# Optimization experiments

Measured on AMD Instinct MI355X. Metric: run time of the kernel, lower is better.

Reference implementation:

```python
import jax, jax.numpy as jnp
import numpy as np

B, N = 64, 8192
RW_APPROX_THRES = 0.6
L_CUTOFF = 100
EPS = 1e-12


def _skew(k):
    kx, ky, kz = k[..., 0], k[..., 1], k[..., 2]
    z = jnp.zeros_like(kx)
    return jnp.stack([
        jnp.stack([z, -kz, ky], -1),
        jnp.stack([kz, z, -kx], -1),
        jnp.stack([-ky, kx, z], -1)], -2)


def so3_exp(v):
    # v: [..., 3] rotation vector -> [..., 3, 3] rotation matrix (Rodrigues)
    theta = jnp.linalg.norm(v, axis=-1, keepdims=True)
    k = v / jnp.maximum(theta, 1e-12)
    K = _skew(k)
    s = jnp.sin(theta)[..., None]
    c = jnp.cos(theta)[..., None]
    I = jnp.eye(3, dtype=v.dtype)
    return I + s * K + (1.0 - c) * (K @ K)


def so3_log(r):
    # r: [..., 3, 3] rotation matrix -> [..., 3] rotation vector
    tr = r[..., 0, 0] + r[..., 1, 1] + r[..., 2, 2]
    cos = jnp.clip((tr - 1.0) * 0.5, -1.0 + 1e-7, 1.0 - 1e-7)
    theta = jnp.arccos(cos)  # [...]
    a = jnp.stack([
        r[..., 2, 1] - r[..., 1, 2],
        r[..., 0, 2] - r[..., 2, 0],
        r[..., 1, 0] - r[..., 0, 1]], axis=-1)  # [..., 3]
    scale = theta / (2.0 * jnp.sin(theta))
    return a * scale[..., None]


def igso3_grad_log_pdf(sigma, omega):
    # sigma: [B], omega: [B, N] angles in (0, pi)
    # f(w) = sum_l (2l+1) exp(-l(l+1) sigma^2 / 2) sin((l+1/2) w) / sin(w/2)
    l = jnp.arange(L_CUTOFF + 1, dtype=omega.dtype)          # [L]
    s2 = (sigma ** 2)[:, None, None]                          # [B,1,1]
    coef = (2.0 * l + 1.0) * jnp.exp(-l * (l + 1.0) * s2 / 2.0)  # [B,1,L]
    w = omega[..., None]                                      # [B,N,1]
    lh = l + 0.5
    sin_h = jnp.sin(w / 2.0)
    cos_h = jnp.cos(w / 2.0)
    sin_lw = jnp.sin(lh * w)                                  # [B,N,L]
    f = jnp.sum(coef * sin_lw / sin_h, axis=-1)               # [B,N]
    df = jnp.sum(coef * (lh * jnp.cos(lh * w) * sin_h - 0.5 * cos_h * sin_lw) / (sin_h ** 2), axis=-1)
    return df / (f + EPS)


def setup_inputs() -> dict:
    key = jax.random.key(0)
    k1, k2, k3, k4, k5 = jax.random.split(key, 5)
    ax1 = jax.random.normal(k1, (B, N, 3), dtype=jnp.float32)
    ax1 = ax1 / jnp.linalg.norm(ax1, axis=-1, keepdims=True)
    ang1 = jax.random.uniform(k2, (B, N, 1), minval=0.1, maxval=3.0, dtype=jnp.float32)
    r_t = so3_exp(ax1 * ang1)
    ax2 = jax.random.normal(k3, (B, N, 3), dtype=jnp.float32)
    ax2 = ax2 / jnp.linalg.norm(ax2, axis=-1, keepdims=True)
    ang2 = jax.random.uniform(k4, (B, N, 1), minval=0.1, maxval=3.0, dtype=jnp.float32)
    rh_0 = so3_exp(ax2 * ang2)
    sigma_t = jax.random.uniform(k5, (B,), minval=0.7, maxval=2.5, dtype=jnp.float32)
    return {"r_t": r_t, "rh_0": rh_0, "sigma_t": sigma_t}


def reference(r_t, rh_0, sigma_t):
    # RotationDiffuser.score with left=True
    r_z = jnp.einsum('bnij,bnkj->bnik', r_t, rh_0)  # r_t @ rh_0^T
    v_z = so3_log(r_z)                               # [B,N,3]
    rw_approx = -v_z / (sigma_t[:, None, None] ** 2)
    w = jnp.linalg.norm(v_z, axis=-1)                # [B,N]
    dlogf_dw = igso3_grad_log_pdf(sigma_t, w)        # [B,N]
    score = jnp.where(sigma_t[:, None, None] > RW_APPROX_THRES,
                      v_z * dlogf_dw[..., None] / (w[..., None] + EPS),
                      rw_approx)
    return score
```

## Files before the change

kernel.cpp:

```cpp
#include <hip/hip_runtime.h>
#include <math.h>


#define BD 256
#define LMAX 100

__device__ __forceinline__ float opq(float x) { __asm__("" : "+v"(x)); return x; }
__device__ __forceinline__ float MULF(float a, float b) { return opq(a * b); }
__device__ __forceinline__ float ADDF(float a, float b) { return opq(a + b); }
__device__ __forceinline__ float SUBF(float a, float b) { return opq(a - b); }
__device__ __forceinline__ float FMAF(float a, float b, float c) { return opq(__builtin_fmaf(a, b, c)); }
__device__ __forceinline__ float DOT3F(float a0, float b0, float a1, float b1,
                                       float a2, float b2) {
    return FMAF(a2, b2, FMAF(a1, b1, MULF(a0, b0)));
}

__device__ __forceinline__ double asin_p(double u) {
    double p = 0.00515311;
    p = __builtin_fma(p, u, 0.00574004);
    p = __builtin_fma(p, u, 0.0064472);
    p = __builtin_fma(p, u, 0.007312526);
    p = __builtin_fma(p, u, 0.008390335809616815);
    p = __builtin_fma(p, u, 0.009761609529194078);
    p = __builtin_fma(p, u, 0.011551800896139706);
    p = __builtin_fma(p, u, 0.01396484375);
    p = __builtin_fma(p, u, 0.017352764423076924);
    p = __builtin_fma(p, u, 0.022372159090909092);
    p = __builtin_fma(p, u, 0.030381944444444444);
    p = __builtin_fma(p, u, 0.044642857142857144);
    p = __builtin_fma(p, u, 0.075);
    p = __builtin_fma(p, u, 0.16666666666666666);
    p = __builtin_fma(p, u, 1.0);
    return p;
}
__device__ __forceinline__ double sin_pd(double u) {
    double p = 2.8114572543455206e-15;
    p = __builtin_fma(p, u, -7.647163731819816e-13);
    p = __builtin_fma(p, u, 1.6059043836821613e-10);
    p = __builtin_fma(p, u, -2.505210838544172e-8);
    p = __builtin_fma(p, u, 2.7557319223985893e-6);
    p = __builtin_fma(p, u, -1.984126984126984e-4);
    p = __builtin_fma(p, u, 8.333333333333333e-3);
    p = __builtin_fma(p, u, -0.16666666666666666);
    p = __builtin_fma(p, u, 1.0);
    return p;
}
__device__ __forceinline__ float sin_pf(float u) {
    float p = -2.5052108e-8f;
    p = __builtin_fmaf(p, u, 2.75573192e-6f);
    p = __builtin_fmaf(p, u, -1.98412698e-4f);
    p = __builtin_fmaf(p, u, 8.33333333e-3f);
    p = __builtin_fmaf(p, u, -0.166666667f);
    p = __builtin_fmaf(p, u, 1.0f);
    return p;
}
__device__ __forceinline__ float cos_pf(float u) {
    float p = 2.08767570e-9f;
    p = __builtin_fmaf(p, u, -2.75573192e-7f);
    p = __builtin_fmaf(p, u, 2.48015873e-5f);
    p = __builtin_fmaf(p, u, -1.38888889e-3f);
    p = __builtin_fmaf(p, u, 4.16666667e-2f);
    p = __builtin_fmaf(p, u, -0.5f);
    p = __builtin_fmaf(p, u, 1.0f);
    return p;
}
__device__ __forceinline__ double exp_d(double x) {
    if (x < -110.0) return 0.0;
    double n = __builtin_rint(x * 1.4426950408889634);
    double r = __builtin_fma(-n, 6.93147180369123816490e-01, x);
    r = __builtin_fma(-n, 1.90821492927058770002e-10, r);
    double p = 2.08767569878681e-9;
    p = __builtin_fma(p, r, 2.505210838544172e-8);
    p = __builtin_fma(p, r, 2.755731922398589e-7);
    p = __builtin_fma(p, r, 2.48015873015873e-5);
    p = __builtin_fma(p, r, 1.984126984126984e-4);
    p = __builtin_fma(p, r, 1.3888888888888889e-3);
    p = __builtin_fma(p, r, 8.333333333333333e-3);
    p = __builtin_fma(p, r, 0.041666666666666664);
    p = __builtin_fma(p, r, 0.16666666666666666);
    p = __builtin_fma(p, r, 0.5);
    p = __builtin_fma(p, r, 1.0);
    p = __builtin_fma(p, r, 1.0);
    long long ni = (long long)n;
    double p2 = __longlong_as_double((1023ll + ni) << 52);
    return p * p2;
}

__global__ __launch_bounds__(BD) void rot_score_kernel(
    const float* __restrict__ rt, const float* __restrict__ rh,
    const float* __restrict__ sigma_t, float* __restrict__ out, int npts)
{
    __shared__ float  sA[BD * 9];
    __shared__ float  sB[BD * 9];
    __shared__ float2 sC[LMAX + 1];

    const int tid = threadIdx.x;
    const int blocksPerB = npts / BD;
    const int b = blockIdx.x / blocksPerB;
    const size_t base = (size_t)blockIdx.x * BD;

    const float sigma = sigma_t[b];
    const float s2 = MULF(sigma, sigma);

    const float* gA = rt + base * 9;
    const float* gB = rh + base * 9;
#pragma unroll
    for (int k = 0; k < 9; ++k) {
        int i = tid + k * BD;
        sA[i] = gA[i];
        sB[i] = gB[i];
    }
    if (tid <= LMAX) {
        float lf = (float)tid;
        float t  = MULF(MULF(-lf, lf + 1.0f), s2);
        float arg = t * 0.5f;
        float e  = (float)exp_d((double)arg);
        float cf = MULF(2.0f * lf + 1.0f, e);
        sC[tid] = make_float2(cf, cf * (lf + 0.5f));
    }
    __syncthreads();

    const int o = tid * 9;
    float a0 = sA[o+0], a1 = sA[o+1], a2 = sA[o+2];
    float a3 = sA[o+3], a4 = sA[o+4], a5 = sA[o+5];
    float a6 = sA[o+6], a7 = sA[o+7], a8 = sA[o+8];
    float b0 = sB[o+0], b1 = sB[o+1], b2 = sB[o+2];
    float b3 = sB[o+3], b4 = sB[o+4], b5 = sB[o+5];
    float b6 = sB[o+6], b7 = sB[o+7], b8 = sB[o+8];

    float m00 = DOT3F(a0,b0, a1,b1, a2,b2);
    float m11 = DOT3F(a3,b3, a4,b4, a5,b5);
    float m22 = DOT3F(a6,b6, a7,b7, a8,b8);
    float m01 = DOT3F(a0,b3, a1,b4, a2,b5);
    float m10 = DOT3F(a3,b0, a4,b1, a5,b2);
    float m02 = DOT3F(a0,b6, a1,b7, a2,b8);
    float m20 = DOT3F(a6,b0, a7,b1, a8,b2);
    float m12 = DOT3F(a3,b6, a4,b7, a5,b8);
    float m21 = DOT3F(a6,b3, a7,b4, a8,b5);

    float tr   = ADDF(ADDF(m00, m11), m22);
    float cosv = MULF(SUBF(tr, 1.0f), 0.5f);
    const float CLO = (float)(-1.0 + 1e-7);
    const float CHI = (float)( 1.0 - 1e-7);
    cosv = fminf(fmaxf(cosv, CLO), CHI);

    double xd = (double)cosv;
    double axd = fabs(xd);
    bool mid = (axd <= 0.5);
    double uedge = (1.0 - axd) * 0.5;
    double m = mid ? xd : sqrt(uedge);
    double asv = m * asin_p(m * m);
    double th_mid  = 1.5707963267948966 - asv;
    double th_edge = (xd > 0.0) ? (2.0 * asv)
                                : (3.141592653589793 - 2.0 * asv);
    double theta_d = mid ? th_mid : th_edge;
    float theta = (float)theta_d;

    double td = (double)theta;
    double e  = (td > 1.5707963267948966) ? (3.141592653589793 - td) : td;
    float st  = (float)(e * sin_pd(e * e));
    float scale = (float)((double)theta / (double)(2.0f * st));
    float ax = SUBF(m21, m12);
    float ay = SUBF(m02, m20);
    float az = SUBF(m10, m01);
    float vx = MULF(ax, scale);
    float vy = MULF(ay, scale);
    float vz = MULF(az, scale);
    float ssum = ADDF(ADDF(MULF(vx,vx), MULF(vy,vy)), MULF(vz,vz));
    float w = (float)sqrt((double)ssum);

    float wh = 0.5f * w;
    float u  = wh * wh;
    float sh = wh * sin_pf(u);
    float ch = cos_pf(u);
    float sw = 2.0f * sh * ch;
    float cw = __builtin_fmaf(-2.0f * sh, sh, 1.0f);

    int nl = (int)ceilf((-1.0f + sqrtf(1.0f + 880.0f / s2)) * 0.5f) + 1;
    if (nl > LMAX + 1) nl = LMAX + 1;

    float s = sh, c = ch;
    float S1 = 0.0f, S2 = 0.0f;
#pragma unroll 2
    for (int l = 0; l < nl; ++l) {
        float2 cc = sC[l];
        S1 = __builtin_fmaf(cc.x, s, S1);
        S2 = __builtin_fmaf(cc.y, c, S2);
        float ns = __builtin_fmaf(s, cw,  c * sw);
        float nc = __builtin_fmaf(c, cw, -(s * sw));
        s = ns; c = nc;
    }
    float num = __builtin_fmaf(S2, sh, -(0.5f * ch * S1));
    float den = __builtin_fmaf(sh, S1, 1e-12f * sh * sh) * (w + 1e-12f);
    float gf  = num / den;

    float ox, oy, oz;
    if (sigma > 0.6f) {
        ox = vx * gf; oy = vy * gf; oz = vz * gf;
    } else {
        float gi = -1.0f / s2;
        ox = vx * gi; oy = vy * gi; oz = vz * gi;
    }

    __syncthreads();
    sA[tid * 3 + 0] = ox;
    sA[tid * 3 + 1] = oy;
    sA[tid * 3 + 2] = oz;
    __syncthreads();
    float* gO = out + base * 3;
#pragma unroll
    for (int k = 0; k < 3; ++k) {
        int i = tid + k * BD;
        gO[i] = sA[i];
    }
}

extern "C" void kernel_launch(void* const* d_in, const int* in_sizes, int n_in,
                              void* d_out, int out_size, void* d_ws, size_t ws_size,
                              hipStream_t stream) {
    const float* r_t     = (const float*)d_in[0];
    const float* rh_0    = (const float*)d_in[1];
    const float* sigma_t = (const float*)d_in[2];
    float* out = (float*)d_out;

    const int nB = in_sizes[2];
    const int n_elem = in_sizes[0] / 9;
    const int npts = n_elem / nB;
    const int grid = n_elem / BD;

    rot_score_kernel<<<grid, BD, 0, stream>>>(r_t, rh_0, sigma_t, out, npts);
}
```

Measured before the change: 80.90 us.

## Vectorize global loads/stores, split recurrence into two chains, drop fp64 ops

Global-to-shared loads and the output store now use float4 accesses instead of scalar strided copies. The Chebyshev-style sine/cosine recurrence is split into two interleaved even/odd chains that step by 2w, which shortens the serial dependency and reads packed float4 coefficients. The fp64 divide and sqrt for scale and w are replaced with float versions. Together these cut memory instruction count and loop latency, at the cost of slightly different rounding in the recurrence and angle math.

```diff
diff --git a/kernel.cpp b/kernel.cpp
--- a/kernel.cpp
+++ b/kernel.cpp
@@ -90,9 +90,9 @@
     const float* __restrict__ rt, const float* __restrict__ rh,
     const float* __restrict__ sigma_t, float* __restrict__ out, int npts)
 {
-    __shared__ float  sA[BD * 9];
-    __shared__ float  sB[BD * 9];
-    __shared__ float2 sC[LMAX + 1];
+    __shared__ __align__(16) float sA[BD * 9];
+    __shared__ __align__(16) float sB[BD * 9];
+    __shared__ float4 sC4[(LMAX + 2) / 2];
 
     const int tid = threadIdx.x;
     const int blocksPerB = npts / BD;
@@ -102,21 +102,25 @@
     const float sigma = sigma_t[b];
     const float s2 = MULF(sigma, sigma);
 
-    const float* gA = rt + base * 9;
-    const float* gB = rh + base * 9;
-#pragma unroll
-    for (int k = 0; k < 9; ++k) {
-        int i = tid + k * BD;
-        sA[i] = gA[i];
-        sB[i] = gB[i];
-    }
-    if (tid <= LMAX) {
+    const float4* gA4 = reinterpret_cast<const float4*>(rt + base * 9);
+    const float4* gB4 = reinterpret_cast<const float4*>(rh + base * 9);
+    float4* sA4 = reinterpret_cast<float4*>(sA);
+    float4* sB4 = reinterpret_cast<float4*>(sB);
+    sA4[tid]      = gA4[tid];
+    sA4[tid + BD] = gA4[tid + BD];
+    sB4[tid]      = gB4[tid];
+    sB4[tid + BD] = gB4[tid + BD];
+    if (tid < 64) {
+        sA4[tid + 2 * BD] = gA4[tid + 2 * BD];
+        sB4[tid + 2 * BD] = gB4[tid + 2 * BD];
+    }
+    if (tid <= LMAX + 1) {
         float lf = (float)tid;
         float t  = MULF(MULF(-lf, lf + 1.0f), s2);
         float arg = t * 0.5f;
         float e  = (float)exp_d((double)arg);
         float cf = MULF(2.0f * lf + 1.0f, e);
-        sC[tid] = make_float2(cf, cf * (lf + 0.5f));
+        ((float2*)sC4)[tid] = make_float2(cf, cf * (lf + 0.5f));
     }
     __syncthreads();
 
@@ -159,7 +163,7 @@
     double td = (double)theta;
     double e  = (td > 1.5707963267948966) ? (3.141592653589793 - td) : td;
     float st  = (float)(e * sin_pd(e * e));
-    float scale = (float)((double)theta / (double)(2.0f * st));
+    float scale = theta / (2.0f * st);
     float ax = SUBF(m21, m12);
     float ay = SUBF(m02, m20);
     float az = SUBF(m10, m01);
@@ -167,7 +171,7 @@
     float vy = MULF(ay, scale);
     float vz = MULF(az, scale);
     float ssum = ADDF(ADDF(MULF(vx,vx), MULF(vy,vy)), MULF(vz,vz));
-    float w = (float)sqrt((double)ssum);
+    float w = sqrtf(ssum);
 
     float wh = 0.5f * w;
     float u  = wh * wh;
@@ -175,21 +179,33 @@
     float ch = cos_pf(u);
     float sw = 2.0f * sh * ch;
     float cw = __builtin_fmaf(-2.0f * sh, sh, 1.0f);
+    float s2w = 2.0f * sw * cw;
+    float c2w = __builtin_fmaf(-2.0f * sw, sw, 1.0f);
 
     int nl = (int)ceilf((-1.0f + sqrtf(1.0f + 880.0f / s2)) * 0.5f) + 1;
     if (nl > LMAX + 1) nl = LMAX + 1;
-
-    float s = sh, c = ch;
-    float S1 = 0.0f, S2 = 0.0f;
+    int nh = (nl + 1) >> 1;
+
+    float sa = sh, ca = ch;
+    float sb = __builtin_fmaf(sh, cw,   ch * sw);
+    float cb = __builtin_fmaf(ch, cw, -(sh * sw));
+    float S1a = 0.0f, S2a = 0.0f, S1b = 0.0f, S2b = 0.0f;
 #pragma unroll 2
-    for (int l = 0; l < nl; ++l) {
-        float2 cc = sC[l];
-        S1 = __builtin_fmaf(cc.x, s, S1);
-        S2 = __builtin_fmaf(cc.y, c, S2);
-        float ns = __builtin_fmaf(s, cw,  c * sw);
-        float nc = __builtin_fmaf(c, cw, -(s * sw));
-        s = ns; c = nc;
-    }
+    for (int j = 0; j < nh; ++j) {
+        float4 q = sC4[j];
+        S1a = __builtin_fmaf(q.x, sa, S1a);
+        S2a = __builtin_fmaf(q.y, ca, S2a);
+        S1b = __builtin_fmaf(q.z, sb, S1b);
+        S2b = __builtin_fmaf(q.w, cb, S2b);
+        float nsa = __builtin_fmaf(sa, c2w,   ca * s2w);
+        float nca = __builtin_fmaf(ca, c2w, -(sa * s2w));
+        float nsb = __builtin_fmaf(sb, c2w,   cb * s2w);
+        float ncb = __builtin_fmaf(cb, c2w, -(sb * s2w));
+        sa = nsa; ca = nca; sb = nsb; cb = ncb;
+    }
+    float S1 = S1a + S1b;
+    float S2 = S2a + S2b;
+
     float num = __builtin_fmaf(S2, sh, -(0.5f * ch * S1));
     float den = __builtin_fmaf(sh, S1, 1e-12f * sh * sh) * (w + 1e-12f);
     float gf  = num / den;
@@ -207,11 +223,9 @@
     sA[tid * 3 + 1] = oy;
     sA[tid * 3 + 2] = oz;
     __syncthreads();
-    float* gO = out + base * 3;
-#pragma unroll
-    for (int k = 0; k < 3; ++k) {
-        int i = tid + k * BD;
-        gO[i] = sA[i];
+    if (tid < (BD * 3) / 4) {
+        float4* gO4 = reinterpret_cast<float4*>(out + base * 3);
+        gO4[tid] = reinterpret_cast<const float4*>(sA)[tid];
     }
 }
 
```

Measured after the change: 82.82 us. 2.4% more time.
